# Performance work log

Measured on AMD Instinct MI355X. Metric: run time of the kernel, lower is better.

Reference implementation:

```python
import jax, jax.numpy as jnp
import numpy as np


def setup_inputs() -> dict:
    key = jax.random.key(0)
    k1, k2 = jax.random.split(key)
    B, N, M = 4, 16384, 4096
    src_points = jax.random.normal(k1, (B, N, 3), dtype=jnp.float32)
    target_verts = jax.random.normal(k2, (B, M, 3), dtype=jnp.float32)
    return {"src_points": src_points, "target_verts": target_verts}


def reference(src_points, target_verts):
    # target_faces=None path of ChamferLoss: degenerate one-vertex triangles,
    # so closest-point-on-mesh == nearest target vertex.
    # d2[b,n,m] = ||p_bn - v_bm||^2 via the expansion p2 + v2 - 2 p.v
    p2 = jnp.sum(src_points * src_points, axis=-1)          # (B, N)
    v2 = jnp.sum(target_verts * target_verts, axis=-1)      # (B, M)
    pv = jnp.einsum('bnd,bmd->bnm', src_points, target_verts)  # (B, N, M)
    d2 = p2[:, :, None] + v2[:, None, :] - 2.0 * pv
    d2 = jnp.maximum(d2, 0.0)
    min_d2 = jnp.min(d2, axis=-1)                            # (B, N)
    num_src_per_batch = src_points.shape[1]
    loss = jnp.sum(min_d2, axis=-1) / num_src_per_batch      # (B,)
    return loss
```

## Files before the change

kernel.cpp:

```cpp
#include <hip/hip_runtime.h>
#include <float.h>


constexpr int B = 4, N = 16384, M = 4096;
constexpr int C   = 16;
constexpr int VC  = M / C;
constexpr int P   = 8;
constexpr int TPB = 256;
constexpr int PPB = TPB * P;
constexpr int PB  = (B * N) / PPB;

__global__ __launch_bounds__(TPB) void chamfer_main(
    const float* __restrict__ src, const float* __restrict__ tv,
    float* __restrict__ partial, float* __restrict__ out)
{
    __shared__ float4 lv[VC];
    const int blk = blockIdx.x;
    const int c   = blk & (C - 1);
    const int pb  = blk >> 4;
    const int b   = pb >> 3;

    if (blk == 0 && threadIdx.x < B) out[threadIdx.x] = 0.0f;

    const float* vsrc = tv + ((size_t)b * M + (size_t)c * VC) * 3;
    for (int i = threadIdx.x; i < VC; i += TPB) {
        float x = vsrc[3 * i + 0];
        float y = vsrc[3 * i + 1];
        float z = vsrc[3 * i + 2];
        lv[i] = make_float4(-2.0f * x, -2.0f * y, -2.0f * z,
                            fmaf(x, x, fmaf(y, y, z * z)));
    }
    __syncthreads();

    const int p0 = pb * PPB + threadIdx.x * P;
    const float* ps = src + (size_t)p0 * 3;
    float px[P], py[P], pz[P], mn[P];
#pragma unroll
    for (int p = 0; p < P; ++p) {
        px[p] = ps[3 * p + 0];
        py[p] = ps[3 * p + 1];
        pz[p] = ps[3 * p + 2];
        mn[p] = FLT_MAX;
    }

#pragma unroll 4
    for (int j = 0; j < VC; ++j) {
        float4 v = lv[j];
#pragma unroll
        for (int p = 0; p < P; ++p) {
            float d = fmaf(v.x, px[p], fmaf(v.y, py[p], fmaf(v.z, pz[p], v.w)));
            mn[p] = fminf(mn[p], d);
        }
    }

#pragma unroll
    for (int p = 0; p < P; ++p) {
        float p2 = fmaf(px[p], px[p], fmaf(py[p], py[p], pz[p] * pz[p]));
        partial[(size_t)(p0 + p) * C + c] = mn[p] + p2;
    }
}

__global__ __launch_bounds__(256) void chamfer_reduce(
    const float* __restrict__ partial, float* __restrict__ out)
{
    const int g = blockIdx.x;
    const int b = g >> 4;
    const int seg = g & 15;
    const int pbase = b * N + seg * 1024;

    float sum = 0.0f;
#pragma unroll
    for (int k = 0; k < 4; ++k) {
        int p = pbase + k * 256 + threadIdx.x;
        const float4* q = (const float4*)(partial + (size_t)p * C);
        float4 a = q[0], d = q[1], e = q[2], f = q[3];
        float m = fminf(
            fminf(fminf(fminf(a.x, a.y), fminf(a.z, a.w)),
                  fminf(fminf(d.x, d.y), fminf(d.z, d.w))),
            fminf(fminf(fminf(e.x, e.y), fminf(e.z, e.w)),
                  fminf(fminf(f.x, f.y), fminf(f.z, f.w))));
        sum += fmaxf(m, 0.0f);
    }

    for (int off = 32; off > 0; off >>= 1)
        sum += __shfl_down(sum, off, 64);
    __shared__ float acc[4];
    if ((threadIdx.x & 63) == 0) acc[threadIdx.x >> 6] = sum;
    __syncthreads();
    if (threadIdx.x == 0) {
        float s = acc[0] + acc[1] + acc[2] + acc[3];
        atomicAdd(&out[b], s * (1.0f / N));
    }
}

extern "C" void kernel_launch(void* const* d_in, const int* in_sizes, int n_in,
                              void* d_out, int out_size, void* d_ws, size_t ws_size,
                              hipStream_t stream) {
    const float* src = (const float*)d_in[0];
    const float* tv  = (const float*)d_in[1];
    float* out = (float*)d_out;
    float* partial = (float*)d_ws;

    chamfer_main<<<PB * C, TPB, 0, stream>>>(src, tv, partial, out);
    chamfer_reduce<<<64, 256, 0, stream>>>(partial, out);
}
```

Baseline: 82.85 us.

## Split targets into 32 chunks, vectorize point loads, transpose partial layout

Doubles the number of target-vertex chunks so the main kernel launches twice as many blocks, each scanning half as many vertices, for better occupancy across CUs. Source points are loaded as float4 vectors, and partial minima are stored chunk-major with float4 stores so writes are coalesced. The reduce kernel now reads coalesced per-chunk rows with one point per thread across more blocks. The cost is double the partial-buffer traffic and more redundant source loads and LDS fills.

Result: no change. 81.58 us (-1.5%).

```diff
diff --git a/kernel.cpp b/kernel.cpp
--- a/kernel.cpp
+++ b/kernel.cpp
@@ -3,12 +3,13 @@
 
 
 constexpr int B = 4, N = 16384, M = 4096;
-constexpr int C   = 16;
+constexpr int BN  = B * N;
+constexpr int C   = 32;
 constexpr int VC  = M / C;
 constexpr int P   = 8;
 constexpr int TPB = 256;
 constexpr int PPB = TPB * P;
-constexpr int PB  = (B * N) / PPB;
+constexpr int PB  = BN / PPB;
 
 __global__ __launch_bounds__(TPB) void chamfer_main(
     const float* __restrict__ src, const float* __restrict__ tv,
@@ -17,7 +18,7 @@
     __shared__ float4 lv[VC];
     const int blk = blockIdx.x;
     const int c   = blk & (C - 1);
-    const int pb  = blk >> 4;
+    const int pb  = blk >> 5;
     const int b   = pb >> 3;
 
     if (blk == 0 && threadIdx.x < B) out[threadIdx.x] = 0.0f;
@@ -33,17 +34,22 @@
     __syncthreads();
 
     const int p0 = pb * PPB + threadIdx.x * P;
-    const float* ps = src + (size_t)p0 * 3;
+    const float4* pv4 = (const float4*)(src + (size_t)p0 * 3);
+    float4 q0 = pv4[0], q1 = pv4[1], q2 = pv4[2],
+           q3 = pv4[3], q4 = pv4[4], q5 = pv4[5];
     float px[P], py[P], pz[P], mn[P];
+    px[0]=q0.x; py[0]=q0.y; pz[0]=q0.z;
+    px[1]=q0.w; py[1]=q1.x; pz[1]=q1.y;
+    px[2]=q1.z; py[2]=q1.w; pz[2]=q2.x;
+    px[3]=q2.y; py[3]=q2.z; pz[3]=q2.w;
+    px[4]=q3.x; py[4]=q3.y; pz[4]=q3.z;
+    px[5]=q3.w; py[5]=q4.x; pz[5]=q4.y;
+    px[6]=q4.z; py[6]=q4.w; pz[6]=q5.x;
+    px[7]=q5.y; py[7]=q5.z; pz[7]=q5.w;
 #pragma unroll
-    for (int p = 0; p < P; ++p) {
-        px[p] = ps[3 * p + 0];
-        py[p] = ps[3 * p + 1];
-        pz[p] = ps[3 * p + 2];
-        mn[p] = FLT_MAX;
-    }
+    for (int p = 0; p < P; ++p) mn[p] = FLT_MAX;
 
-#pragma unroll 4
+#pragma unroll 8
     for (int j = 0; j < VC; ++j) {
         float4 v = lv[j];
 #pragma unroll
@@ -53,34 +59,27 @@
         }
     }
 
+    float o[P];
 #pragma unroll
     for (int p = 0; p < P; ++p) {
         float p2 = fmaf(px[p], px[p], fmaf(py[p], py[p], pz[p] * pz[p]));
-        partial[(size_t)(p0 + p) * C + c] = mn[p] + p2;
+        o[p] = mn[p] + p2;
     }
+    float4* dst = (float4*)(partial + (size_t)c * BN + p0);
+    dst[0] = make_float4(o[0], o[1], o[2], o[3]);
+    dst[1] = make_float4(o[4], o[5], o[6], o[7]);
 }
 
 __global__ __launch_bounds__(256) void chamfer_reduce(
     const float* __restrict__ partial, float* __restrict__ out)
 {
-    const int g = blockIdx.x;
-    const int b = g >> 4;
-    const int seg = g & 15;
-    const int pbase = b * N + seg * 1024;
+    const int p = blockIdx.x * 256 + threadIdx.x;
+    const int b = blockIdx.x >> 6;
 
-    float sum = 0.0f;
+    float m = FLT_MAX;
 #pragma unroll
-    for (int k = 0; k < 4; ++k) {
-        int p = pbase + k * 256 + threadIdx.x;
-        const float4* q = (const float4*)(partial + (size_t)p * C);
-        float4 a = q[0], d = q[1], e = q[2], f = q[3];
-        float m = fminf(
-            fminf(fminf(fminf(a.x, a.y), fminf(a.z, a.w)),
-                  fminf(fminf(d.x, d.y), fminf(d.z, d.w))),
-            fminf(fminf(fminf(e.x, e.y), fminf(e.z, e.w)),
-                  fminf(fminf(f.x, f.y), fminf(f.z, f.w))));
-        sum += fmaxf(m, 0.0f);
-    }
+    for (int c = 0; c < C; ++c) m = fminf(m, partial[(size_t)c * BN + p]);
+    float sum = fmaxf(m, 0.0f);
 
     for (int off = 32; off > 0; off >>= 1)
         sum += __shfl_down(sum, off, 64);
@@ -102,5 +101,5 @@
     float* partial = (float*)d_ws;
 
     chamfer_main<<<PB * C, TPB, 0, stream>>>(src, tv, partial, out);
-    chamfer_reduce<<<64, 256, 0, stream>>>(partial, out);
+    chamfer_reduce<<<256, 256, 0, stream>>>(partial, out);
 }
```
